# Kernel optimization log

Hardware: AMD Instinct MI355X
Metric: run time of the kernel (lower is better)

Reference implementation:

```python
import jax, jax.numpy as jnp
import numpy as np

N_NODES = 50000
N_EDGES = 1600000
F_IN = 128
HID = 32
HEADS = 4
N_CLS = 2
NEG_SLOPE = 0.2


def gat_conv(x, src, dst, W, a_src, a_dst, b, heads, ch, n):
    # x: [N, F_in]; W: [F_in, heads*ch]; a_src/a_dst: [heads, ch]; b: [heads*ch]
    h = (x @ W).reshape(n, heads, ch)                      # [N, H, C]
    alpha_s = jnp.einsum('nhc,hc->nh', h, a_src)           # [N, H]
    alpha_d = jnp.einsum('nhc,hc->nh', h, a_dst)           # [N, H]
    e = jax.nn.leaky_relu(alpha_s[src] + alpha_d[dst], NEG_SLOPE)  # [E, H]
    m = jax.ops.segment_max(e, dst, num_segments=n)        # [N, H]
    ex = jnp.exp(e - m[dst])                               # [E, H]
    denom = jax.ops.segment_sum(ex, dst, num_segments=n)   # [N, H]
    alpha = ex / denom[dst]                                # [E, H]
    msg = h[src] * alpha[:, :, None]                       # [E, H, C]
    out = jax.ops.segment_sum(msg, dst, num_segments=n)    # [N, H, C]
    return out.reshape(n, heads * ch) + b


def setup_inputs() -> dict:
    key = jax.random.key(0)
    ks = jax.random.split(key, 16)
    g = lambda k, shp, fan: jax.random.normal(k, shp, jnp.float32) * (1.0 / np.sqrt(fan))
    x = jax.random.normal(ks[0], (N_NODES, F_IN), jnp.float32)
    edge_index = jax.random.randint(ks[1], (2, N_EDGES), 0, N_NODES, jnp.int32)
    return {
        'x': x,
        'edge_index': edge_index,
        'W1': g(ks[2], (F_IN, HEADS * HID), F_IN),
        'a1s': g(ks[3], (HEADS, HID), HID),
        'a1d': g(ks[4], (HEADS, HID), HID),
        'b1': jnp.zeros((HEADS * HID,), jnp.float32),
        'W2': g(ks[5], (HEADS * HID, HEADS * HID), HEADS * HID),
        'a2s': g(ks[6], (HEADS, HID), HID),
        'a2d': g(ks[7], (HEADS, HID), HID),
        'b2': jnp.zeros((HEADS * HID,), jnp.float32),
        'W3': g(ks[8], (HEADS * HID, HID), HEADS * HID),
        'a3s': g(ks[9], (1, HID), HID),
        'a3d': g(ks[10], (1, HID), HID),
        'b3': jnp.zeros((HID,), jnp.float32),
        'Wlin': g(ks[11], (HID, N_CLS), HID),
        'blin': jnp.zeros((N_CLS,), jnp.float32),
    }


def reference(x, edge_index, W1, a1s, a1d, b1, W2, a2s, a2d, b2, W3, a3s, a3d, b3, Wlin, blin):
    n = x.shape[0]
    # PyG GATConv default: add self-loops
    loop = jnp.arange(n, dtype=edge_index.dtype)
    src = jnp.concatenate([edge_index[0], loop])
    dst = jnp.concatenate([edge_index[1], loop])
    h = gat_conv(x, src, dst, W1, a1s, a1d, b1, HEADS, HID, n)
    h = jax.nn.relu(h)
    h = gat_conv(h, src, dst, W2, a2s, a2d, b2, HEADS, HID, n)
    h = jax.nn.relu(h)
    h = gat_conv(h, src, dst, W3, a3s, a3d, b3, 1, HID, n)
    h = jax.nn.relu(h)
    return h @ Wlin + blin
```

## Files before the change

### kernel.cpp

```cpp
#include <hip/hip_runtime.h>

#define NEG 0.2f
#define BSH 8
#define CHB 8192
__device__ __forceinline__ float lrelu(float x){ return fmaxf(x, NEG*x); }

__device__ __forceinline__ float bf2f(unsigned short u){
  union{unsigned int i; float f;} v; v.i = ((unsigned int)u)<<16; return v.f;
}
__device__ __forceinline__ unsigned short f2bf(float f){
  union{float f; unsigned int i;} v; v.f = f;
  unsigned int b = v.i;
  b += 0x7FFFu + ((b>>16)&1u);
  return (unsigned short)(b>>16);
}

__global__ __launch_bounds__(256) void zero_kernel(int* __restrict__ p, int n){
  int i = blockIdx.x*256 + threadIdx.x;
  if (i < n) p[i] = 0;
}

__global__ __launch_bounds__(256) void bin_count(const int* __restrict__ dstv, int* __restrict__ bcnt,
                                                 int E, int NB){
  __shared__ int lh[256];
  int tid = threadIdx.x;
  lh[tid] = 0;
  __syncthreads();
  int e0 = blockIdx.x * CHB;
  int e1 = min(e0 + CHB, E);
  for (int i = e0 + tid; i < e1; i += 256)
    atomicAdd(&lh[dstv[i] >> BSH], 1);
  __syncthreads();
  if (tid < NB && lh[tid] > 0) atomicAdd(&bcnt[tid], lh[tid]);
}

__global__ __launch_bounds__(256) void scan_kernel(const int* __restrict__ counts, int* __restrict__ offs,
                                                   int* __restrict__ cursor, int n){
  __shared__ int wsum[4];
  __shared__ int carry_s;
  int tid = threadIdx.x, lane = tid & 63, wv = tid >> 6;
  if (tid == 0) carry_s = 0;
  __syncthreads();
  const int CH = 2048;
  int nch = (n + CH - 1)/CH;
  for (int ch=0; ch<nch; ++ch){
    int base_i = ch*CH + tid*8;
    int v[8], pre[8];
    #pragma unroll
    for (int j=0;j<8;++j){ int i=base_i+j; v[j]=(i<n)?counts[i]:0; }
    int t=0;
    #pragma unroll
    for (int j=0;j<8;++j){ pre[j]=t; t+=v[j]; }
    int incl=t;
    #pragma unroll
    for (int m=1;m<64;m<<=1){ int u=__shfl_up(incl,m); if(lane>=m) incl+=u; }
    int wexcl = incl - t;
    if (lane==63) wsum[wv]=incl;
    __syncthreads();
    int wbase=0;
    for (int w2=0;w2<wv;++w2) wbase+=wsum[w2];
    int total = wsum[0]+wsum[1]+wsum[2]+wsum[3];
    int base = carry_s + wbase + wexcl;
    #pragma unroll
    for (int j=0;j<8;++j){ int i=base_i+j; if(i<n){ int val=base+pre[j]; offs[i]=val; cursor[i]=val; } }
    __syncthreads();
    if (tid==0) carry_s += total;
    __syncthreads();
  }
  if (tid==0) offs[n]=carry_s;
}

__global__ __launch_bounds__(256) void bin_scatter(const int* __restrict__ srcv, const int* __restrict__ dstv,
                                                   int* __restrict__ bcur, int2* __restrict__ pairs,
                                                   int E, int NB){
  __shared__ int lh[256];
  __shared__ int lcur[256];
  int tid = threadIdx.x;
  lh[tid] = 0;
  __syncthreads();
  int e0 = blockIdx.x * CHB;
  int e1 = min(e0 + CHB, E);
  for (int i = e0 + tid; i < e1; i += 256)
    atomicAdd(&lh[dstv[i] >> BSH], 1);
  __syncthreads();
  if (tid < NB){
    int c = lh[tid];
    lcur[tid] = (c > 0) ? atomicAdd(&bcur[tid], c) : 0;
  }
  __syncthreads();
  for (int i = e0 + tid; i < e1; i += 256){
    int s = srcv[i], d = dstv[i];
    int p = atomicAdd(&lcur[d >> BSH], 1);
    pairs[p] = make_int2(s, d);
  }
}

__global__ __launch_bounds__(256) void bucket_finalize(const int2* __restrict__ pairs,
                                                       const int* __restrict__ bbase,
                                                       int* __restrict__ offs, int* __restrict__ csr,
                                                       int N, int E){
  __shared__ int lh[256];
  __shared__ int lcur[256];
  __shared__ int wsum[4];
  int b = blockIdx.x;
  int base = bbase[b], end = bbase[b+1];
  int node0 = b << BSH;
  int tid = threadIdx.x, lane = tid & 63, wv = tid >> 6;
  lh[tid] = 0;
  if (b == 0 && tid == 0) offs[N] = E;
  __syncthreads();
  for (int i = base + tid; i < end; i += 256)
    atomicAdd(&lh[pairs[i].y - node0], 1);
  __syncthreads();
  {
    int v = lh[tid];
    int incl = v;
    #pragma unroll
    for (int m=1;m<64;m<<=1){ int u=__shfl_up(incl,m); if(lane>=m) incl+=u; }
    if (lane==63) wsum[wv]=incl;
    __syncthreads();
    int wbase=0;
    for (int w2=0;w2<wv;++w2) wbase+=wsum[w2];
    int excl = wbase + incl - v;
    lcur[tid] = base + excl;
    int node = node0 + tid;
    if (node < N) offs[node] = base + excl;
  }
  __syncthreads();
  for (int i = base + tid; i < end; i += 256){
    int2 pr = pairs[i];
    int p = atomicAdd(&lcur[pr.y - node0], 1);
    csr[p] = pr.x;
  }
}

template<int NOUT, int HEADS>
__global__ __launch_bounds__(256) void gemm_fused(const float* __restrict__ X, const float* __restrict__ W,
    const float* __restrict__ a_s, const float* __restrict__ a_d,
    unsigned short* __restrict__ hb, float* __restrict__ as_, float* __restrict__ ad_, int n){
  constexpr int NC = NOUT / 8;
  constexpr int RG = 256 / NC;
  constexpr int BM = RG * 8;
  __shared__ float Wl[128 * NOUT];
  for (int i = threadIdx.x; i < 128*NOUT/4; i += 256)
    ((float4*)Wl)[i] = ((const float4*)W)[i];
  __syncthreads();
  int cg = threadIdx.x % NC;
  int rg = threadIdx.x / NC;
  int lane = threadIdx.x & 63;
  int row0 = blockIdx.x * BM + rg * 8;
  float acc[8][8];
  #pragma unroll
  for (int r=0;r<8;++r)
    #pragma unroll
    for (int c=0;c<8;++c) acc[r][c]=0.f;
  for (int k4 = 0; k4 < 32; ++k4){
    float4 xv[8];
    #pragma unroll
    for (int r = 0; r < 8; ++r){
      int row = row0 + r;
      xv[r] = (row < n) ? ((const float4*)(X + (size_t)row*128))[k4] : make_float4(0.f,0.f,0.f,0.f);
    }
    #pragma unroll
    for (int kk = 0; kk < 4; ++kk){
      int k = k4*4 + kk;
      float wv[8];
      #pragma unroll
      for (int c = 0; c < 8; ++c) wv[c] = Wl[k*NOUT + cg*8 + c];
      #pragma unroll
      for (int r = 0; r < 8; ++r){
        float xr = (kk==0)?xv[r].x:(kk==1)?xv[r].y:(kk==2)?xv[r].z:xv[r].w;
        #pragma unroll
        for (int c = 0; c < 8; ++c) acc[r][c] = fmaf(xr, wv[c], acc[r][c]);
      }
    }
  }
  float asl[8], adl[8];
  #pragma unroll
  for (int c=0;c<8;++c){ asl[c]=a_s[cg*8+c]; adl[c]=a_d[cg*8+c]; }
  #pragma unroll
  for (int r = 0; r < 8; ++r){
    int row = row0 + r;
    float s=0.f, dd=0.f;
    #pragma unroll
    for (int c=0;c<8;++c){ s = fmaf(acc[r][c], asl[c], s); dd = fmaf(acc[r][c], adl[c], dd); }
    s  += __shfl_xor(s,1);  s  += __shfl_xor(s,2);
    dd += __shfl_xor(dd,1); dd += __shfl_xor(dd,2);
    if (HEADS == 4){
      int base = lane & ~15;
      float s0=__shfl(s,base),  s1=__shfl(s,base+4),  s2=__shfl(s,base+8),  s3=__shfl(s,base+12);
      float d0=__shfl(dd,base), d1=__shfl(dd,base+4), d2=__shfl(dd,base+8), d3=__shfl(dd,base+12);
      if (row < n && cg == 0){
        ((float4*)as_)[row] = make_float4(s0,s1,s2,s3);
        ((float4*)ad_)[row] = make_float4(d0,d1,d2,d3);
      }
    } else {
      if (row < n && (lane&3) == 0){ as_[row] = s; ad_[row] = dd; }
    }
    if (row < n){
      ushort4 p0, p1;
      p0.x=f2bf(acc[r][0]); p0.y=f2bf(acc[r][1]); p0.z=f2bf(acc[r][2]); p0.w=f2bf(acc[r][3]);
      p1.x=f2bf(acc[r][4]); p1.y=f2bf(acc[r][5]); p1.z=f2bf(acc[r][6]); p1.w=f2bf(acc[r][7]);
      *(ushort4*)&hb[(size_t)row*NOUT + cg*8 + 0] = p0;
      *(ushort4*)&hb[(size_t)row*NOUT + cg*8 + 4] = p1;
    }
  }
}

__device__ __forceinline__ float sel4(int hh, float4 v){
  return (hh&2) ? ((hh&1)?v.w:v.z) : ((hh&1)?v.y:v.x);
}

__global__ __launch_bounds__(256) void agg_h4(const unsigned short* __restrict__ hb,
    const float4* __restrict__ as_, const float4* __restrict__ ad_,
    const int* __restrict__ offs, const int* __restrict__ csr,
    const float* __restrict__ bias, float* __restrict__ hout, int n){
  int wid = (blockIdx.x*256 + threadIdx.x) >> 6;
  int lane = threadIdx.x & 63;
  if (wid >= n) return;
  const int d = wid;
  float4 ad4 = ad_[d];
  float4 asd = as_[d];
  int r0 = offs[d], r1 = offs[d+1];
  int half = lane >> 5;
  int cl = lane & 31;
  int hh = cl >> 3;
  float adh = sel4(hh, ad4);
  float asv = sel4(hh, asd);
  float acc0=0.f, acc1=0.f, acc2=0.f, acc3=0.f, den=0.f;
  if (half == 0){
    float w = __expf(lrelu(asv+adh));
    ushort4 hv = *(const ushort4*)&hb[(size_t)d*128 + 4*cl];
    acc0 = w*bf2f(hv.x); acc1 = w*bf2f(hv.y); acc2 = w*bf2f(hv.z); acc3 = w*bf2f(hv.w); den = w;
  }
  int e = r0 + half;
  for (; e+14 < r1; e += 16){
    int s0=csr[e],   s1=csr[e+2],  s2=csr[e+4],  s3=csr[e+6];
    int s4=csr[e+8], s5=csr[e+10], s6=csr[e+12], s7=csr[e+14];
    float4 a0=as_[s0], a1=as_[s1], a2=as_[s2], a3=as_[s3];
    float4 a4=as_[s4], a5=as_[s5], a6=as_[s6], a7=as_[s7];
    ushort4 h0=*(const ushort4*)&hb[(size_t)s0*128+4*cl];
    ushort4 h1=*(const ushort4*)&hb[(size_t)s1*128+4*cl];
    ushort4 h2=*(const ushort4*)&hb[(size_t)s2*128+4*cl];
    ushort4 h3=*(const ushort4*)&hb[(size_t)s3*128+4*cl];
    ushort4 h4=*(const ushort4*)&hb[(size_t)s4*128+4*cl];
    ushort4 h5=*(const ushort4*)&hb[(size_t)s5*128+4*cl];
    ushort4 h6=*(const ushort4*)&hb[(size_t)s6*128+4*cl];
    ushort4 h7=*(const ushort4*)&hb[(size_t)s7*128+4*cl];
    float w0=__expf(lrelu(sel4(hh,a0)+adh));
    float w1=__expf(lrelu(sel4(hh,a1)+adh));
    float w2=__expf(lrelu(sel4(hh,a2)+adh));
    float w3=__expf(lrelu(sel4(hh,a3)+adh));
    float w4=__expf(lrelu(sel4(hh,a4)+adh));
    float w5=__expf(lrelu(sel4(hh,a5)+adh));
    float w6=__expf(lrelu(sel4(hh,a6)+adh));
    float w7=__expf(lrelu(sel4(hh,a7)+adh));
    acc0=fmaf(w0,bf2f(h0.x),acc0); acc1=fmaf(w0,bf2f(h0.y),acc1); acc2=fmaf(w0,bf2f(h0.z),acc2); acc3=fmaf(w0,bf2f(h0.w),acc3); den+=w0;
    acc0=fmaf(w1,bf2f(h1.x),acc0); acc1=fmaf(w1,bf2f(h1.y),acc1); acc2=fmaf(w1,bf2f(h1.z),acc2); acc3=fmaf(w1,bf2f(h1.w),acc3); den+=w1;
    acc0=fmaf(w2,bf2f(h2.x),acc0); acc1=fmaf(w2,bf2f(h2.y),acc1); acc2=fmaf(w2,bf2f(h2.z),acc2); acc3=fmaf(w2,bf2f(h2.w),acc3); den+=w2;
    acc0=fmaf(w3,bf2f(h3.x),acc0); acc1=fmaf(w3,bf2f(h3.y),acc1); acc2=fmaf(w3,bf2f(h3.z),acc2); acc3=fmaf(w3,bf2f(h3.w),acc3); den+=w3;
    acc0=fmaf(w4,bf2f(h4.x),acc0); acc1=fmaf(w4,bf2f(h4.y),acc1); acc2=fmaf(w4,bf2f(h4.z),acc2); acc3=fmaf(w4,bf2f(h4.w),acc3); den+=w4;
    acc0=fmaf(w5,bf2f(h5.x),acc0); acc1=fmaf(w5,bf2f(h5.y),acc1); acc2=fmaf(w5,bf2f(h5.z),acc2); acc3=fmaf(w5,bf2f(h5.w),acc3); den+=w5;
    acc0=fmaf(w6,bf2f(h6.x),acc0); acc1=fmaf(w6,bf2f(h6.y),acc1); acc2=fmaf(w6,bf2f(h6.z),acc2); acc3=fmaf(w6,bf2f(h6.w),acc3); den+=w6;
    acc0=fmaf(w7,bf2f(h7.x),acc0); acc1=fmaf(w7,bf2f(h7.y),acc1); acc2=fmaf(w7,bf2f(h7.z),acc2); acc3=fmaf(w7,bf2f(h7.w),acc3); den+=w7;
  }
  for (; e < r1; e += 2){
    int s = csr[e];
    float4 a4 = as_[s];
    float w = __expf(lrelu(sel4(hh,a4)+adh));
    ushort4 hv = *(const ushort4*)&hb[(size_t)s*128+4*cl];
    acc0=fmaf(w,bf2f(hv.x),acc0); acc1=fmaf(w,bf2f(hv.y),acc1); acc2=fmaf(w,bf2f(hv.z),acc2); acc3=fmaf(w,bf2f(hv.w),acc3); den+=w;
  }
  acc0 += __shfl_xor(acc0,32); acc1 += __shfl_xor(acc1,32);
  acc2 += __shfl_xor(acc2,32); acc3 += __shfl_xor(acc3,32);
  den  += __shfl_xor(den,32);
  if (half == 0){
    float inv = 1.0f/den;
    float4 bv = *(const float4*)&bias[4*cl];
    float4 o;
    o.x = fmaxf(fmaf(acc0,inv,bv.x), 0.f);
    o.y = fmaxf(fmaf(acc1,inv,bv.y), 0.f);
    o.z = fmaxf(fmaf(acc2,inv,bv.z), 0.f);
    o.w = fmaxf(fmaf(acc3,inv,bv.w), 0.f);
    *(float4*)&hout[(size_t)d*128 + 4*cl] = o;
  }
}

__global__ __launch_bounds__(256) void agg_h1_lin(const unsigned short* __restrict__ hb,
    const float* __restrict__ as_, const float* __restrict__ ad_,
    const int* __restrict__ offs, const int* __restrict__ csr,
    const float* __restrict__ b3, const float* __restrict__ Wlin, const float* __restrict__ blin,
    float* __restrict__ out, int n){
  int wid = (blockIdx.x*256 + threadIdx.x) >> 6;
  int lane = threadIdx.x & 63;
  if (wid >= n) return;
  const int d = wid;
  float add = ad_[d];
  float asd = as_[d];
  int r0 = offs[d], r1 = offs[d+1];
  int half = lane >> 5;
  int c = lane & 31;
  float acc=0.f, den=0.f;
  if (half == 0){
    float w = __expf(lrelu(asd+add));
    acc = w*bf2f(hb[(size_t)d*32 + c]); den = w;
  }
  int e = r0 + half;
  for (; e+14 < r1; e += 16){
    int s0=csr[e],   s1=csr[e+2],  s2=csr[e+4],  s3=csr[e+6];
    int s4=csr[e+8], s5=csr[e+10], s6=csr[e+12], s7=csr[e+14];
    float a0=as_[s0], a1=as_[s1], a2=as_[s2], a3=as_[s3];
    float a4=as_[s4], a5=as_[s5], a6=as_[s6], a7=as_[s7];
    float v0=bf2f(hb[(size_t)s0*32+c]), v1=bf2f(hb[(size_t)s1*32+c]);
    float v2=bf2f(hb[(size_t)s2*32+c]), v3=bf2f(hb[(size_t)s3*32+c]);
    float v4=bf2f(hb[(size_t)s4*32+c]), v5=bf2f(hb[(size_t)s5*32+c]);
    float v6=bf2f(hb[(size_t)s6*32+c]), v7=bf2f(hb[(size_t)s7*32+c]);
    float w0=__expf(lrelu(a0+add)), w1=__expf(lrelu(a1+add));
    float w2=__expf(lrelu(a2+add)), w3=__expf(lrelu(a3+add));
    float w4=__expf(lrelu(a4+add)), w5=__expf(lrelu(a5+add));
    float w6=__expf(lrelu(a6+add)), w7=__expf(lrelu(a7+add));
    acc=fmaf(w0,v0,acc); den+=w0;
    acc=fmaf(w1,v1,acc); den+=w1;
    acc=fmaf(w2,v2,acc); den+=w2;
    acc=fmaf(w3,v3,acc); den+=w3;
    acc=fmaf(w4,v4,acc); den+=w4;
    acc=fmaf(w5,v5,acc); den+=w5;
    acc=fmaf(w6,v6,acc); den+=w6;
    acc=fmaf(w7,v7,acc); den+=w7;
  }
  for (; e < r1; e += 2){
    int s = csr[e];
    float w=__expf(lrelu(as_[s]+add));
    acc=fmaf(w,bf2f(hb[(size_t)s*32+c]),acc); den+=w;
  }
  acc += __shfl_xor(acc,32);
  den += __shfl_xor(den,32);
  float v = fmaxf(acc/den + b3[c], 0.f);
  float y0 = v*Wlin[c*2+0];
  float y1 = v*Wlin[c*2+1];
  #pragma unroll
  for (int mk=16; mk>=1; mk>>=1){ y0 += __shfl_xor(y0,mk); y1 += __shfl_xor(y1,mk); }
  if (lane==0){ out[(size_t)d*2+0] = y0 + blin[0]; out[(size_t)d*2+1] = y1 + blin[1]; }
}

extern "C" void kernel_launch(void* const* d_in, const int* in_sizes, int n_in,
                              void* d_out, int out_size, void* d_ws, size_t ws_size,
                              hipStream_t stream){
  const int N = in_sizes[0] / 128;
  const int E = in_sizes[1] / 2;
  const float* x    = (const float*)d_in[0];
  const int*   ei   = (const int*)d_in[1];
  const int*   srcv = ei;
  const int*   dstv = ei + E;
  const float* W1 = (const float*)d_in[2];
  const float* a1s= (const float*)d_in[3];
  const float* a1d= (const float*)d_in[4];
  const float* b1 = (const float*)d_in[5];
  const float* W2 = (const float*)d_in[6];
  const float* a2s= (const float*)d_in[7];
  const float* a2d= (const float*)d_in[8];
  const float* b2 = (const float*)d_in[9];
  const float* W3 = (const float*)d_in[10];
  const float* a3s= (const float*)d_in[11];
  const float* a3d= (const float*)d_in[12];
  const float* b3 = (const float*)d_in[13];
  const float* Wlin=(const float*)d_in[14];
  const float* blin=(const float*)d_in[15];
  float* out = (float*)d_out;

  const int NB = (N + 255) >> BSH;

  char* wp = (char*)d_ws;
  auto alloc = [&](size_t bytes)->void*{
    void* p = (void*)wp;
    wp += (bytes + 255) & ~(size_t)255;
    return p;
  };
  float* h     = (float*)alloc((size_t)N*128*4);
  unsigned short* hb = (unsigned short*)alloc((size_t)N*128*2);
  float* as_   = (float*)alloc((size_t)N*4*4);
  float* ad_   = (float*)alloc((size_t)N*4*4);
  int*   offs  = (int*)alloc((size_t)(N+1)*4);
  int*   csr   = (int*)alloc((size_t)E*4);
  int*   bcnt  = (int*)alloc((size_t)NB*4);
  int*   bbase = (int*)alloc((size_t)(NB+1)*4);
  int*   bcur  = (int*)alloc((size_t)NB*4);
  int2*  pairs = (int2*)h;

  const int gridB = (E + CHB - 1)/CHB;
  const int gridW = (N + 3)/4;

  zero_kernel<<<1, 256, 0, stream>>>(bcnt, NB);
  bin_count<<<gridB, 256, 0, stream>>>(dstv, bcnt, E, NB);
  scan_kernel<<<1, 256, 0, stream>>>(bcnt, bbase, bcur, NB);
  bin_scatter<<<gridB, 256, 0, stream>>>(srcv, dstv, bcur, pairs, E, NB);
  bucket_finalize<<<NB, 256, 0, stream>>>(pairs, bbase, offs, csr, N, E);

  gemm_fused<128,4><<<(N+127)/128, 256, 0, stream>>>(x, W1, a1s, a1d, hb, as_, ad_, N);
  agg_h4<<<gridW, 256, 0, stream>>>(hb, (const float4*)as_, (const float4*)ad_, offs, csr, b1, h, N);

  gemm_fused<128,4><<<(N+127)/128, 256, 0, stream>>>(h, W2, a2s, a2d, hb, as_, ad_, N);
  agg_h4<<<gridW, 256, 0, stream>>>(hb, (const float4*)as_, (const float4*)ad_, offs, csr, b2, h, N);

  gemm_fused<32,1><<<(N+511)/512, 256, 0, stream>>>(h, W3, a3s, a3d, hb, as_, ad_, N);
  agg_h1_lin<<<gridW, 256, 0, stream>>>(hb, as_, ad_, offs, csr, b3, Wlin, blin, out, N);
}
```

Measured before the change: 489.0 us.

## Split GAT aggregation per head with head-major features and precomputed edge weights

The GEMM now stores bf16 features in a head-major layout, one N×32 plane per head, so each per-head gather touches a smaller working set that fits better in cache. A new edge kernel precomputes the exp(leaky_relu) attention weight for all four heads per CSR edge, using a new per-edge destination array. Aggregation then runs as four per-head launches, each processing four edges at a time across the wavefront. In exchange it adds writes and reads of a 16-byte-per-edge weight buffer, reads the CSR four times per layer, and adds kernel launches.

```diff
diff --git a/kernel.cpp b/kernel.cpp
--- a/kernel.cpp
+++ b/kernel.cpp
@@ -98,6 +98,7 @@
 __global__ __launch_bounds__(256) void bucket_finalize(const int2* __restrict__ pairs,
                                                        const int* __restrict__ bbase,
                                                        int* __restrict__ offs, int* __restrict__ csr,
+                                                       int* __restrict__ csrd,
                                                        int N, int E){
   __shared__ int lh[256];
   __shared__ int lcur[256];
@@ -131,6 +132,7 @@
     int2 pr = pairs[i];
     int p = atomicAdd(&lcur[pr.y - node0], 1);
     csr[p] = pr.x;
+    csrd[p] = pr.y;
   }
 }
 
@@ -201,88 +203,68 @@
       ushort4 p0, p1;
       p0.x=f2bf(acc[r][0]); p0.y=f2bf(acc[r][1]); p0.z=f2bf(acc[r][2]); p0.w=f2bf(acc[r][3]);
       p1.x=f2bf(acc[r][4]); p1.y=f2bf(acc[r][5]); p1.z=f2bf(acc[r][6]); p1.w=f2bf(acc[r][7]);
-      *(ushort4*)&hb[(size_t)row*NOUT + cg*8 + 0] = p0;
-      *(ushort4*)&hb[(size_t)row*NOUT + cg*8 + 4] = p1;
-    }
-  }
-}
-
-__device__ __forceinline__ float sel4(int hh, float4 v){
-  return (hh&2) ? ((hh&1)?v.w:v.z) : ((hh&1)?v.y:v.x);
-}
-
-__global__ __launch_bounds__(256) void agg_h4(const unsigned short* __restrict__ hb,
+      size_t baseo = (size_t)(cg>>2)*((size_t)n*32) + (size_t)row*32 + (size_t)(cg&3)*8;
+      *(ushort4*)&hb[baseo + 0] = p0;
+      *(ushort4*)&hb[baseo + 4] = p1;
+    }
+  }
+}
+
+__global__ __launch_bounds__(256) void edge_w4(const int* __restrict__ csr, const int* __restrict__ csrd,
     const float4* __restrict__ as_, const float4* __restrict__ ad_,
-    const int* __restrict__ offs, const int* __restrict__ csr,
-    const float* __restrict__ bias, float* __restrict__ hout, int n){
+    float* __restrict__ wT, int E){
+  int e = blockIdx.x*256 + threadIdx.x;
+  if (e >= E) return;
+  int s = csr[e], d = csrd[e];
+  float4 a = as_[s], b = ad_[d];
+  wT[e]             = __expf(lrelu(a.x+b.x));
+  wT[(size_t)E+e]   = __expf(lrelu(a.y+b.y));
+  wT[(size_t)2*E+e] = __expf(lrelu(a.z+b.z));
+  wT[(size_t)3*E+e] = __expf(lrelu(a.w+b.w));
+}
+
+__global__ __launch_bounds__(256) void agg_head(const unsigned short* __restrict__ hbh,
+    const float* __restrict__ asf, const float* __restrict__ adf, int hsel,
+    const float* __restrict__ wh, const int* __restrict__ offs, const int* __restrict__ csr,
+    const float* __restrict__ biash, float* __restrict__ houtb, int n){
   int wid = (blockIdx.x*256 + threadIdx.x) >> 6;
   int lane = threadIdx.x & 63;
   if (wid >= n) return;
   const int d = wid;
-  float4 ad4 = ad_[d];
-  float4 asd = as_[d];
+  int q = lane >> 4;
+  int cl = lane & 15;
   int r0 = offs[d], r1 = offs[d+1];
-  int half = lane >> 5;
-  int cl = lane & 31;
-  int hh = cl >> 3;
-  float adh = sel4(hh, ad4);
-  float asv = sel4(hh, asd);
-  float acc0=0.f, acc1=0.f, acc2=0.f, acc3=0.f, den=0.f;
-  if (half == 0){
-    float w = __expf(lrelu(asv+adh));
-    ushort4 hv = *(const ushort4*)&hb[(size_t)d*128 + 4*cl];
-    acc0 = w*bf2f(hv.x); acc1 = w*bf2f(hv.y); acc2 = w*bf2f(hv.z); acc3 = w*bf2f(hv.w); den = w;
-  }
-  int e = r0 + half;
-  for (; e+14 < r1; e += 16){
-    int s0=csr[e],   s1=csr[e+2],  s2=csr[e+4],  s3=csr[e+6];
-    int s4=csr[e+8], s5=csr[e+10], s6=csr[e+12], s7=csr[e+14];
-    float4 a0=as_[s0], a1=as_[s1], a2=as_[s2], a3=as_[s3];
-    float4 a4=as_[s4], a5=as_[s5], a6=as_[s6], a7=as_[s7];
-    ushort4 h0=*(const ushort4*)&hb[(size_t)s0*128+4*cl];
-    ushort4 h1=*(const ushort4*)&hb[(size_t)s1*128+4*cl];
-    ushort4 h2=*(const ushort4*)&hb[(size_t)s2*128+4*cl];
-    ushort4 h3=*(const ushort4*)&hb[(size_t)s3*128+4*cl];
-    ushort4 h4=*(const ushort4*)&hb[(size_t)s4*128+4*cl];
-    ushort4 h5=*(const ushort4*)&hb[(size_t)s5*128+4*cl];
-    ushort4 h6=*(const ushort4*)&hb[(size_t)s6*128+4*cl];
-    ushort4 h7=*(const ushort4*)&hb[(size_t)s7*128+4*cl];
-    float w0=__expf(lrelu(sel4(hh,a0)+adh));
-    float w1=__expf(lrelu(sel4(hh,a1)+adh));
-    float w2=__expf(lrelu(sel4(hh,a2)+adh));
-    float w3=__expf(lrelu(sel4(hh,a3)+adh));
-    float w4=__expf(lrelu(sel4(hh,a4)+adh));
-    float w5=__expf(lrelu(sel4(hh,a5)+adh));
-    float w6=__expf(lrelu(sel4(hh,a6)+adh));
-    float w7=__expf(lrelu(sel4(hh,a7)+adh));
-    acc0=fmaf(w0,bf2f(h0.x),acc0); acc1=fmaf(w0,bf2f(h0.y),acc1); acc2=fmaf(w0,bf2f(h0.z),acc2); acc3=fmaf(w0,bf2f(h0.w),acc3); den+=w0;
-    acc0=fmaf(w1,bf2f(h1.x),acc0); acc1=fmaf(w1,bf2f(h1.y),acc1); acc2=fmaf(w1,bf2f(h1.z),acc2); acc3=fmaf(w1,bf2f(h1.w),acc3); den+=w1;
-    acc0=fmaf(w2,bf2f(h2.x),acc0); acc1=fmaf(w2,bf2f(h2.y),acc1); acc2=fmaf(w2,bf2f(h2.z),acc2); acc3=fmaf(w2,bf2f(h2.w),acc3); den+=w2;
-    acc0=fmaf(w3,bf2f(h3.x),acc0); acc1=fmaf(w3,bf2f(h3.y),acc1); acc2=fmaf(w3,bf2f(h3.z),acc2); acc3=fmaf(w3,bf2f(h3.w),acc3); den+=w3;
-    acc0=fmaf(w4,bf2f(h4.x),acc0); acc1=fmaf(w4,bf2f(h4.y),acc1); acc2=fmaf(w4,bf2f(h4.z),acc2); acc3=fmaf(w4,bf2f(h4.w),acc3); den+=w4;
-    acc0=fmaf(w5,bf2f(h5.x),acc0); acc1=fmaf(w5,bf2f(h5.y),acc1); acc2=fmaf(w5,bf2f(h5.z),acc2); acc3=fmaf(w5,bf2f(h5.w),acc3); den+=w5;
-    acc0=fmaf(w6,bf2f(h6.x),acc0); acc1=fmaf(w6,bf2f(h6.y),acc1); acc2=fmaf(w6,bf2f(h6.z),acc2); acc3=fmaf(w6,bf2f(h6.w),acc3); den+=w6;
-    acc0=fmaf(w7,bf2f(h7.x),acc0); acc1=fmaf(w7,bf2f(h7.y),acc1); acc2=fmaf(w7,bf2f(h7.z),acc2); acc3=fmaf(w7,bf2f(h7.w),acc3); den+=w7;
-  }
-  for (; e < r1; e += 2){
-    int s = csr[e];
-    float4 a4 = as_[s];
-    float w = __expf(lrelu(sel4(hh,a4)+adh));
-    ushort4 hv = *(const ushort4*)&hb[(size_t)s*128+4*cl];
-    acc0=fmaf(w,bf2f(hv.x),acc0); acc1=fmaf(w,bf2f(hv.y),acc1); acc2=fmaf(w,bf2f(hv.z),acc2); acc3=fmaf(w,bf2f(hv.w),acc3); den+=w;
-  }
-  acc0 += __shfl_xor(acc0,32); acc1 += __shfl_xor(acc1,32);
-  acc2 += __shfl_xor(acc2,32); acc3 += __shfl_xor(acc3,32);
-  den  += __shfl_xor(den,32);
-  if (half == 0){
+  float acc0=0.f, acc1=0.f, den=0.f;
+  if (q == 0){
+    float w = __expf(lrelu(asf[4*d+hsel] + adf[4*d+hsel]));
+    unsigned int hv = *(const unsigned int*)&hbh[(size_t)d*32 + 2*cl];
+    acc0 = w*bf2f((unsigned short)(hv&0xffffu));
+    acc1 = w*bf2f((unsigned short)(hv>>16));
+    den = w;
+  }
+  for (int base = r0; base < r1; base += 16){
+    #pragma unroll
+    for (int j = 0; j < 4; ++j){
+      int e = base + j*4 + q;
+      bool v = e < r1;
+      int ee = v ? e : r0;
+      int s = csr[ee];
+      float w = v ? wh[ee] : 0.f;
+      unsigned int hv = *(const unsigned int*)&hbh[(size_t)s*32 + 2*cl];
+      acc0 = fmaf(w, bf2f((unsigned short)(hv&0xffffu)), acc0);
+      acc1 = fmaf(w, bf2f((unsigned short)(hv>>16)), acc1);
+      den += w;
+    }
+  }
+  acc0 += __shfl_xor(acc0,16); acc0 += __shfl_xor(acc0,32);
+  acc1 += __shfl_xor(acc1,16); acc1 += __shfl_xor(acc1,32);
+  den  += __shfl_xor(den,16);  den  += __shfl_xor(den,32);
+  if (q == 0){
     float inv = 1.0f/den;
-    float4 bv = *(const float4*)&bias[4*cl];
-    float4 o;
-    o.x = fmaxf(fmaf(acc0,inv,bv.x), 0.f);
-    o.y = fmaxf(fmaf(acc1,inv,bv.y), 0.f);
-    o.z = fmaxf(fmaf(acc2,inv,bv.z), 0.f);
-    o.w = fmaxf(fmaf(acc3,inv,bv.w), 0.f);
-    *(float4*)&hout[(size_t)d*128 + 4*cl] = o;
+    float2 o;
+    o.x = fmaxf(fmaf(acc0, inv, biash[2*cl  ]), 0.f);
+    o.y = fmaxf(fmaf(acc1, inv, biash[2*cl+1]), 0.f);
+    *(float2*)&houtb[(size_t)d*128 + 2*cl] = o;
   }
 }
 
@@ -382,25 +364,34 @@
   float* ad_   = (float*)alloc((size_t)N*4*4);
   int*   offs  = (int*)alloc((size_t)(N+1)*4);
   int*   csr   = (int*)alloc((size_t)E*4);
+  int*   csrd  = (int*)alloc((size_t)E*4);
+  float* wT    = (float*)alloc((size_t)E*4*4);
   int*   bcnt  = (int*)alloc((size_t)NB*4);
   int*   bbase = (int*)alloc((size_t)(NB+1)*4);
   int*   bcur  = (int*)alloc((size_t)NB*4);
   int2*  pairs = (int2*)h;
 
   const int gridB = (E + CHB - 1)/CHB;
+  const int gridE = (E + 255)/256;
   const int gridW = (N + 3)/4;
 
   zero_kernel<<<1, 256, 0, stream>>>(bcnt, NB);
   bin_count<<<gridB, 256, 0, stream>>>(dstv, bcnt, E, NB);
   scan_kernel<<<1, 256, 0, stream>>>(bcnt, bbase, bcur, NB);
   bin_scatter<<<gridB, 256, 0, stream>>>(srcv, dstv, bcur, pairs, E, NB);
-  bucket_finalize<<<NB, 256, 0, stream>>>(pairs, bbase, offs, csr, N, E);
+  bucket_finalize<<<NB, 256, 0, stream>>>(pairs, bbase, offs, csr, csrd, N, E);
 
   gemm_fused<128,4><<<(N+127)/128, 256, 0, stream>>>(x, W1, a1s, a1d, hb, as_, ad_, N);
-  agg_h4<<<gridW, 256, 0, stream>>>(hb, (const float4*)as_, (const float4*)ad_, offs, csr, b1, h, N);
+  edge_w4<<<gridE, 256, 0, stream>>>(csr, csrd, (const float4*)as_, (const float4*)ad_, wT, E);
+  for (int hh = 0; hh < 4; ++hh)
+    agg_head<<<gridW, 256, 0, stream>>>(hb + (size_t)hh*N*32, as_, ad_, hh,
+                                        wT + (size_t)hh*E, offs, csr, b1 + 32*hh, h + 32*hh, N);
 
   gemm_fused<128,4><<<(N+127)/128, 256, 0, stream>>>(h, W2, a2s, a2d, hb, as_, ad_, N);
-  agg_h4<<<gridW, 256, 0, stream>>>(hb, (const float4*)as_, (const float4*)ad_, offs, csr, b2, h, N);
+  edge_w4<<<gridE, 256, 0, stream>>>(csr, csrd, (const float4*)as_, (const float4*)ad_, wT, E);
+  for (int hh = 0; hh < 4; ++hh)
+    agg_head<<<gridW, 256, 0, stream>>>(hb + (size_t)hh*N*32, as_, ad_, hh,
+                                        wT + (size_t)hh*E, offs, csr, b2 + 32*hh, h + 32*hh, N);
 
   gemm_fused<32,1><<<(N+511)/512, 256, 0, stream>>>(h, W3, a3s, a3d, hb, as_, ad_, N);
   agg_h1_lin<<<gridW, 256, 0, stream>>>(hb, as_, ad_, offs, csr, b3, Wlin, blin, out, N);
```

Result: slower. 604.5 us (+23.6%).
